# Optimization experiments

Hardware: AMD Instinct MI355X
Metric: run time of the kernel (lower is better)

## Reference

```python
import jax, jax.numpy as jnp
import numpy as np

N_EMBD = 768
N_HEAD = 12
HEAD_DIM = N_EMBD // N_HEAD


def setup_inputs() -> dict:
    key = jax.random.key(0)
    k0, k1, k2, k3, k4 = jax.random.split(key, 5)
    B, T, C = 2, 4096, N_EMBD
    x = jax.random.normal(k0, (B, T, C), dtype=jnp.float32)
    # c_attn: Linear(C, 3C); c_proj: Linear(C, C). torch Linear: y = x @ W.T + b
    s = 1.0 / np.sqrt(C)
    W_attn = jax.random.uniform(k1, (3 * C, C), dtype=jnp.float32, minval=-s, maxval=s)
    b_attn = jax.random.uniform(k2, (3 * C,), dtype=jnp.float32, minval=-s, maxval=s)
    W_proj = jax.random.uniform(k3, (C, C), dtype=jnp.float32, minval=-s, maxval=s)
    b_proj = jax.random.uniform(k4, (C,), dtype=jnp.float32, minval=-s, maxval=s)
    return {"x": x, "W_attn": W_attn, "b_attn": b_attn, "W_proj": W_proj, "b_proj": b_proj}


def reference(x, W_attn, b_attn, W_proj, b_proj):
    B, T, C = x.shape
    H, D = N_HEAD, HEAD_DIM
    qkv = x @ W_attn.T + b_attn                      # [B,T,3C]
    q, k, v = jnp.split(qkv, 3, axis=-1)
    # [B,T,C] -> [B,H,T,D]
    q = q.reshape(B, T, H, D).transpose(0, 2, 1, 3)
    k = k.reshape(B, T, H, D).transpose(0, 2, 1, 3)
    v = v.reshape(B, T, H, D).transpose(0, 2, 1, 3)
    scale = 1.0 / jnp.sqrt(jnp.asarray(D, dtype=x.dtype))
    att = jnp.einsum('bhqd,bhkd->bhqk', q, k) * scale  # [B,H,T,T]
    att = jax.nn.softmax(att, axis=-1)
    y = jnp.einsum('bhqk,bhkd->bhqd', att, v)          # [B,H,T,D]
    y = y.transpose(0, 2, 1, 3).reshape(B, T, C)
    return y @ W_proj.T + b_proj
```

## Files before the change

### kernel.cpp

```cpp
#include <hip/hip_runtime.h>
#include <stdint.h>
#include <stddef.h>

typedef __bf16 bf16_t;
typedef bf16_t bf16x4 __attribute__((ext_vector_type(4)));
typedef bf16_t bf16x8 __attribute__((ext_vector_type(8)));
typedef float  f32x4  __attribute__((ext_vector_type(4)));
typedef _Float16 f16_t;
typedef f16_t f16x2 __attribute__((ext_vector_type(2)));
typedef f16_t f16x4 __attribute__((ext_vector_type(4)));
typedef __fp16 fp16x2_raw __attribute__((ext_vector_type(2)));

__device__ __forceinline__ f16x2 pkrtz(float a, float b) {
    fp16x2_raw r = __builtin_amdgcn_cvt_pkrtz(a, b);
    union { fp16x2_raw r; f16x2 h; } u;
    u.r = r;
    return u.h;
}

#define MFMA_BF16_K32(a, b, c) __builtin_amdgcn_mfma_f32_16x16x32_bf16(a, b, c, 0, 0, 0)
#define MFMA_F16_K16(a, b, c)  __builtin_amdgcn_mfma_f32_16x16x16f16(a, b, c, 0, 0, 0)

__device__ __forceinline__ void gload_lds16(const void* g, void* l) {
    __builtin_amdgcn_global_load_lds(
        (const __attribute__((address_space(1))) void*)g,
        (__attribute__((address_space(3))) void*)l,
        16, 0, 0);
}

#define NX 1572864
#define NWA 442368
#define NWP 147456
__global__ void cvt_all(const float* __restrict__ x, const float* __restrict__ Wa,
                        const float* __restrict__ Wp, bf16_t* __restrict__ xb,
                        bf16_t* __restrict__ Wab, bf16_t* __restrict__ Wpb) {
    int i = blockIdx.x * blockDim.x + threadIdx.x;
    const float4* src; bf16_t* dst; int j;
    if (i < NX)            { src = (const float4*)x;  dst = xb;  j = i; }
    else if (i < NX + NWA) { src = (const float4*)Wa; dst = Wab; j = i - NX; }
    else                   { src = (const float4*)Wp; dst = Wpb; j = i - NX - NWA; }
    float4 f = src[j];
    bf16x4 o = { (bf16_t)f.x, (bf16_t)f.y, (bf16_t)f.z, (bf16_t)f.w };
    ((bf16x4*)dst)[j] = o;
}

template <int KDIM>
__device__ __forceinline__ void gemm_mainloop(
    const bf16_t* __restrict__ A, const bf16_t* __restrict__ Bt,
    bf16_t* As, bf16_t* Bs, int m0, int n0, int wave, int lane, f32x4 acc[4][4])
{
    const int quad = lane >> 4, l15 = lane & 15;
    const int wm = ((wave >> 1) << 6), wn = ((wave & 1) << 6);

    const int srow = (wave << 4) + (lane >> 2);
    const int sw   = (((lane & 3) ^ ((srow >> 1) & 3)) << 3);
    const bf16_t* gA = A  + (size_t)(m0 + srow) * KDIM + sw;
    const bf16_t* gB = Bt + (size_t)(n0 + srow) * KDIM + sw;
    bf16_t* lA0 = As + wave * 512;
    bf16_t* lA1 = As + 2048 + wave * 512;
    bf16_t* lB0 = Bs + wave * 512;
    bf16_t* lB1 = Bs + 2048 + wave * 512;

    const int xorv = ((quad ^ ((l15 >> 1) & 3)) << 3);

    for (int k0 = 0; k0 < KDIM; k0 += 32) {
        __syncthreads();
        gload_lds16(gA + k0,                       lA0);
        gload_lds16(gA + (size_t)64 * KDIM + k0,   lA1);
        gload_lds16(gB + k0,                       lB0);
        gload_lds16(gB + (size_t)64 * KDIM + k0,   lB1);
        __syncthreads();

        bf16x8 af[4], bfr[4];
#pragma unroll
        for (int t = 0; t < 4; t++) {
            af[t]  = *(const bf16x8*)(As + (wm + t * 16 + l15) * 32 + xorv);
            bfr[t] = *(const bf16x8*)(Bs + (wn + t * 16 + l15) * 32 + xorv);
        }
#pragma unroll
        for (int mt = 0; mt < 4; mt++)
#pragma unroll
            for (int nt = 0; nt < 4; nt++)
                acc[mt][nt] = MFMA_BF16_K32(af[mt], bfr[nt], acc[mt][nt]);
    }
}

__global__ __launch_bounds__(256) void gemm_qkv(
    const bf16_t* __restrict__ A,
    const bf16_t* __restrict__ Bt,
    const float* __restrict__ bias,
    bf16_t* __restrict__ qo, bf16_t* __restrict__ ko, f16_t* __restrict__ vo)
{
    __shared__ bf16_t As[128 * 32];
    __shared__ bf16_t Bs[128 * 32];
    const int tid = threadIdx.x, wave = tid >> 6, lane = tid & 63;
    const int quad = lane >> 4, l15 = lane & 15;
    const int m0 = blockIdx.y * 128, n0 = blockIdx.x * 128;
    f32x4 acc[4][4] = {};
    gemm_mainloop<768>(A, Bt, As, Bs, m0, n0, wave, lane, acc);

    const int wm = ((wave >> 1) << 6), wn = ((wave & 1) << 6);
#pragma unroll
    for (int nt = 0; nt < 4; nt++) {
        const int cc = n0 + wn + nt * 16 + l15;
        const float bia = bias[cc];
        const int which = cc / 768;
        const int rem = cc - which * 768;
        const int h = rem >> 6, d = rem & 63;
        if (which < 2) {
            bf16_t* dst = (which == 0) ? qo : ko;
#pragma unroll
            for (int mt = 0; mt < 4; mt++) {
#pragma unroll
                for (int r = 0; r < 4; r++) {
                    const int row = m0 + wm + mt * 16 + quad * 4 + r;
                    const int b = row >> 12, t = row & 4095;
                    dst[((size_t)(b * 12 + h) * 4096 + t) * 64 + d] =
                        (bf16_t)(acc[mt][nt][r] + bia);
                }
            }
        } else {
#pragma unroll
            for (int mt = 0; mt < 4; mt++) {
                const int row0 = m0 + wm + mt * 16 + quad * 4;
                const int b = row0 >> 12, t0 = row0 & 4095;
                f16x4 ov = { (f16_t)(acc[mt][nt][0] + bia),
                             (f16_t)(acc[mt][nt][1] + bia),
                             (f16_t)(acc[mt][nt][2] + bia),
                             (f16_t)(acc[mt][nt][3] + bia) };
                *(f16x4*)(vo + ((size_t)(b * 12 + h) * 64 + d) * 4096 + t0) = ov;
            }
        }
    }
}

__global__ __launch_bounds__(256) void gemm_proj(
    const bf16_t* __restrict__ A,
    const bf16_t* __restrict__ Bt,
    const float* __restrict__ bias,
    float* __restrict__ out)
{
    __shared__ bf16_t As[128 * 32];
    __shared__ bf16_t Bs[128 * 32];
    const int tid = threadIdx.x, wave = tid >> 6, lane = tid & 63;
    const int quad = lane >> 4, l15 = lane & 15;
    const int m0 = blockIdx.y * 128, n0 = blockIdx.x * 128;
    f32x4 acc[4][4] = {};
    gemm_mainloop<768>(A, Bt, As, Bs, m0, n0, wave, lane, acc);

    const int wm = ((wave >> 1) << 6), wn = ((wave & 1) << 6);
#pragma unroll
    for (int nt = 0; nt < 4; nt++) {
        const int cc = n0 + wn + nt * 16 + l15;
        const float bia = bias[cc];
#pragma unroll
        for (int mt = 0; mt < 4; mt++) {
#pragma unroll
            for (int r = 0; r < 4; r++) {
                const int row = m0 + wm + mt * 16 + quad * 4 + r;
                out[(size_t)row * 768 + cc] = acc[mt][nt][r] + bia;
            }
        }
    }
}

#define QSCALE 0.1803368801f
__global__ __launch_bounds__(256, 3) void attn_fwd(
    const bf16_t* __restrict__ qg, const bf16_t* __restrict__ kg,
    const f16_t* __restrict__ vtg, bf16_t* __restrict__ y)
{
    __shared__ __align__(16) char smem[36608];
    bf16_t* Ks0 = (bf16_t*)(smem);
    bf16_t* Ks1 = (bf16_t*)(smem + 8192);
    f16_t*  Vt0 = (f16_t*)(smem + 16384);
    f16_t*  Vt1 = (f16_t*)(smem + 24576);
    float*  RedA = (float*)(smem);
    float*  RedB = (float*)(smem + 17408);
    float*  Psr  = (float*)(smem + 34816);
    float*  PsT  = (float*)(smem + 35840);

    const int tid = threadIdx.x, wave = tid >> 6, lane = tid & 63;
    const int quad = lane >> 4, l15 = lane & 15;

    const int blk = blockIdx.x;
    const int xcd = blk & 7;
    const int idx = blk >> 3;
    const int hl  = idx % 3;
    const int qt  = idx / 3;
    const int bh  = xcd * 3 + hl;
    const int b = bh / 12, h = bh - b * 12;
    const size_t base = (size_t)bh * 4096 * 64;

    bf16x8 qf[4][2];
#pragma unroll
    for (int qc = 0; qc < 4; qc++) {
        const int qrow = qt * 64 + qc * 16 + l15;
        qf[qc][0] = *(const bf16x8*)(qg + base + (size_t)qrow * 64 + quad * 8);
        qf[qc][1] = *(const bf16x8*)(qg + base + (size_t)qrow * 64 + 32 + quad * 8);
#pragma unroll
        for (int j = 0; j < 8; j++) {
            qf[qc][0][j] = (bf16_t)((float)qf[qc][0][j] * QSCALE);
            qf[qc][1][j] = (bf16_t)((float)qf[qc][1][j] * QSCALE);
        }
    }

    f32x4 O[4][4] = {};
    float psum[4] = {};
    const f16x2 one2 = { (f16_t)1.0f, (f16_t)1.0f };

    const int srow8 = tid >> 3;
    const int sc8   = (tid & 7) ^ (srow8 & 7);
    const int l8 = l15 & 7;
    const int w16 = wave << 4;
    const int ksoff = (quad ^ l8) << 3;
    const int vslot = ((wave << 1) | (quad >> 1)) ^ l8;
    const int q0off = (quad & 1) * 8;

    auto stage = [&](const bf16_t* kp, const f16_t* vp, bf16_t* Kd, f16_t* Vd) {
#pragma unroll
        for (int i = 0; i < 2; i++) {
            gload_lds16(kp + (i * 32 + srow8) * 64 + sc8 * 8,           Kd + (i * 256 + tid) * 8);
            gload_lds16(vp + (size_t)(i * 32 + srow8) * 4096 + sc8 * 8, Vd + (i * 256 + tid) * 8);
        }
    };

    auto compute = [&](const bf16_t* ks, const f16_t* vs) {
        const bf16_t* kr = ks + (w16 + l15) * 64;
        bf16x8 kf0 = *(const bf16x8*)(kr + ksoff);
        bf16x8 kf1 = *(const bf16x8*)(kr + (ksoff ^ 32));
        f32x4 sc[4];
#pragma unroll
        for (int qc = 0; qc < 4; qc++) {
            f32x4 s = {};
            s = MFMA_BF16_K32(kf0, qf[qc][0], s);
            s = MFMA_BF16_K32(kf1, qf[qc][1], s);
            sc[qc] = s;
        }
        f16x4 pf[4];
#pragma unroll
        for (int qc = 0; qc < 4; qc++) {
            float e0 = __builtin_amdgcn_exp2f(sc[qc][0]);
            float e1 = __builtin_amdgcn_exp2f(sc[qc][1]);
            float e2 = __builtin_amdgcn_exp2f(sc[qc][2]);
            float e3 = __builtin_amdgcn_exp2f(sc[qc][3]);
            f16x2 lo = pkrtz(e0, e1);
            f16x2 hi = pkrtz(e2, e3);
            psum[qc] = __builtin_amdgcn_fdot2(lo, one2, psum[qc], false);
            psum[qc] = __builtin_amdgcn_fdot2(hi, one2, psum[qc], false);
            f16x4 p;
            *(f16x2*)&p = lo;
            *(((f16x2*)&p) + 1) = hi;
            pf[qc] = p;
        }
#pragma unroll
        for (int dt = 0; dt < 4; dt++) {
            const char* vr = (const char*)(vs + (dt * 16 + l15) * 64);
            f16x4 vf = *(const f16x4*)(vr + vslot * 16 + q0off);
#pragma unroll
            for (int qc = 0; qc < 4; qc++)
                O[dt][qc] = MFMA_F16_K16(vf, pf[qc], O[dt][qc]);
        }
    };

    const bf16_t* kp = kg + base;
    const f16_t*  vp = vtg + base;
    stage(kp, vp, Ks0, Vt0); kp += 4096; vp += 64;
    for (int kt = 0; kt < 64; kt += 2) {
        __syncthreads();
        stage(kp, vp, Ks1, Vt1); kp += 4096; vp += 64;
        compute(Ks0, Vt0);
        __syncthreads();
        if (kt + 2 < 64) { stage(kp, vp, Ks0, Vt0); kp += 4096; vp += 64; }
        compute(Ks1, Vt1);
    }

#pragma unroll
    for (int qc = 0; qc < 4; qc++) {
        psum[qc] += __shfl_xor(psum[qc], 16, 64);
        psum[qc] += __shfl_xor(psum[qc], 32, 64);
    }
    __syncthreads();
    if (wave == 2) {
#pragma unroll
        for (int dt = 0; dt < 4; dt++)
#pragma unroll
            for (int qc = 0; qc < 4; qc++)
                *(f32x4*)(RedA + (qc * 16 + l15) * 68 + dt * 16 + quad * 4) = O[dt][qc];
    } else if (wave == 3) {
#pragma unroll
        for (int dt = 0; dt < 4; dt++)
#pragma unroll
            for (int qc = 0; qc < 4; qc++)
                *(f32x4*)(RedB + (qc * 16 + l15) * 68 + dt * 16 + quad * 4) = O[dt][qc];
    }
    if (quad == 0) {
#pragma unroll
        for (int qc = 0; qc < 4; qc++) Psr[wave * 64 + qc * 16 + l15] = psum[qc];
    }
    __syncthreads();
    if (wave == 0) {
#pragma unroll
        for (int dt = 0; dt < 4; dt++)
#pragma unroll
            for (int qc = 0; qc < 4; qc++)
                O[dt][qc] += *(const f32x4*)(RedA + (qc * 16 + l15) * 68 + dt * 16 + quad * 4);
    } else if (wave == 1) {
#pragma unroll
        for (int dt = 0; dt < 4; dt++)
#pragma unroll
            for (int qc = 0; qc < 4; qc++)
                O[dt][qc] += *(const f32x4*)(RedB + (qc * 16 + l15) * 68 + dt * 16 + quad * 4);
    }
    __syncthreads();
    if (wave == 1) {
#pragma unroll
        for (int dt = 0; dt < 4; dt++)
#pragma unroll
            for (int qc = 0; qc < 4; qc++)
                *(f32x4*)(RedA + (qc * 16 + l15) * 68 + dt * 16 + quad * 4) = O[dt][qc];
    } else if (wave == 3) {
        PsT[lane] = Psr[lane] + Psr[64 + lane] + Psr[128 + lane] + Psr[192 + lane];
    }
    __syncthreads();
    if (wave == 0) {
#pragma unroll
        for (int qc = 0; qc < 4; qc++) {
            const float rcp = 1.0f / PsT[qc * 16 + l15];
            const int t = qt * 64 + qc * 16 + l15;
            bf16_t* yr = y + ((size_t)b * 4096 + t) * 768 + h * 64 + quad * 4;
#pragma unroll
            for (int dt = 0; dt < 4; dt++) {
                f32x4 o4 = O[dt][qc] +
                    *(const f32x4*)(RedA + (qc * 16 + l15) * 68 + dt * 16 + quad * 4);
                bf16x4 ov = { (bf16_t)(o4[0] * rcp), (bf16_t)(o4[1] * rcp),
                              (bf16_t)(o4[2] * rcp), (bf16_t)(o4[3] * rcp) };
                *(bf16x4*)(yr + dt * 16) = ov;
            }
        }
    }
}

extern "C" void kernel_launch(void* const* d_in, const int* in_sizes, int n_in,
                              void* d_out, int out_size, void* d_ws, size_t ws_size,
                              hipStream_t stream) {
    const float* x  = (const float*)d_in[0];
    const float* Wa = (const float*)d_in[1];
    const float* ba = (const float*)d_in[2];
    const float* Wp = (const float*)d_in[3];
    const float* bp = (const float*)d_in[4];
    float* out = (float*)d_out;

    char* ws = (char*)d_ws;
    bf16_t* xb  = (bf16_t*)(ws);
    bf16_t* Wab = (bf16_t*)(ws + 12582912);
    bf16_t* Wpb = (bf16_t*)(ws + 16121856);
    bf16_t* qb  = (bf16_t*)(ws + 17301504);
    bf16_t* kb  = (bf16_t*)(ws + 29884416);
    f16_t*  vtb = (f16_t*)(ws + 42467328);
    bf16_t* yb  = (bf16_t*)(ws + 55050240);

    cvt_all<<<8448, 256, 0, stream>>>(x, Wa, Wp, xb, Wab, Wpb);
    gemm_qkv <<<dim3(18, 64), 256, 0, stream>>>(xb, Wab, ba, qb, kb, vtb);
    attn_fwd <<<1536, 256, 0, stream>>>(qb, kb, vtb, yb);
    gemm_proj<<<dim3( 6, 64), 256, 0, stream>>>(yb, Wpb, bp, out);
}
```

Measured before the change: 277.7 us.

## Triple-buffer attention K/V staging and transpose GEMM operands for vector stores

The attention kernel moves from double to triple-buffered K/V tiles in LDS, using explicit vmcnt waits plus a raw s_barrier so the copy for tile t+2 stays in flight while tile t is computed. Both GEMMs swap operands (weights as A, activations as B), so each lane owns four consecutive output features and can write bf16x4, float4 or strided f16 stores and read bias as a float4. The extra buffer raises LDS use per block, which may limit occupancy under the 3-blocks-per-CU bound. The V-transpose epilogue now uses scalar strided stores instead of f16x4.

```diff
diff --git a/kernel.cpp b/kernel.cpp
--- a/kernel.cpp
+++ b/kernel.cpp
@@ -86,8 +86,8 @@
 }
 
 __global__ __launch_bounds__(256) void gemm_qkv(
-    const bf16_t* __restrict__ A,
-    const bf16_t* __restrict__ Bt,
+    const bf16_t* __restrict__ Wab,
+    const bf16_t* __restrict__ xb,
     const float* __restrict__ bias,
     bf16_t* __restrict__ qo, bf16_t* __restrict__ ko, f16_t* __restrict__ vo)
 {
@@ -95,48 +95,43 @@
     __shared__ bf16_t Bs[128 * 32];
     const int tid = threadIdx.x, wave = tid >> 6, lane = tid & 63;
     const int quad = lane >> 4, l15 = lane & 15;
-    const int m0 = blockIdx.y * 128, n0 = blockIdx.x * 128;
+    const int m0 = blockIdx.x * 128;
+    const int n0 = blockIdx.y * 128;
     f32x4 acc[4][4] = {};
-    gemm_mainloop<768>(A, Bt, As, Bs, m0, n0, wave, lane, acc);
+    gemm_mainloop<768>(Wab, xb, As, Bs, m0, n0, wave, lane, acc);
 
     const int wm = ((wave >> 1) << 6), wn = ((wave & 1) << 6);
 #pragma unroll
     for (int nt = 0; nt < 4; nt++) {
-        const int cc = n0 + wn + nt * 16 + l15;
-        const float bia = bias[cc];
-        const int which = cc / 768;
-        const int rem = cc - which * 768;
-        const int h = rem >> 6, d = rem & 63;
-        if (which < 2) {
-            bf16_t* dst = (which == 0) ? qo : ko;
-#pragma unroll
-            for (int mt = 0; mt < 4; mt++) {
-#pragma unroll
-                for (int r = 0; r < 4; r++) {
-                    const int row = m0 + wm + mt * 16 + quad * 4 + r;
-                    const int b = row >> 12, t = row & 4095;
-                    dst[((size_t)(b * 12 + h) * 4096 + t) * 64 + d] =
-                        (bf16_t)(acc[mt][nt][r] + bia);
-                }
+        const int tok = n0 + wn + nt * 16 + l15;
+        const int b = tok >> 12, tt = tok & 4095;
+#pragma unroll
+        for (int mt = 0; mt < 4; mt++) {
+            const int f0 = m0 + wm + mt * 16 + quad * 4;
+            const float4 bi = *(const float4*)(bias + f0);
+            const int which = f0 / 768;
+            const int rem = f0 - which * 768;
+            const int h = rem >> 6, d0 = rem & 63;
+            const float v0 = acc[mt][nt][0] + bi.x, v1 = acc[mt][nt][1] + bi.y;
+            const float v2 = acc[mt][nt][2] + bi.z, v3 = acc[mt][nt][3] + bi.w;
+            if (which < 2) {
+                bf16_t* dst = (which == 0) ? qo : ko;
+                bf16x4 ov = { (bf16_t)v0, (bf16_t)v1, (bf16_t)v2, (bf16_t)v3 };
+                *(bf16x4*)(dst + ((size_t)(b * 12 + h) * 4096 + tt) * 64 + d0) = ov;
+            } else {
+                f16_t* vd = vo + ((size_t)(b * 12 + h) * 64 + d0) * 4096 + tt;
+                vd[0]         = (f16_t)v0;
+                vd[4096]      = (f16_t)v1;
+                vd[2 * 4096]  = (f16_t)v2;
+                vd[3 * 4096]  = (f16_t)v3;
             }
-        } else {
-#pragma unroll
-            for (int mt = 0; mt < 4; mt++) {
-                const int row0 = m0 + wm + mt * 16 + quad * 4;
-                const int b = row0 >> 12, t0 = row0 & 4095;
-                f16x4 ov = { (f16_t)(acc[mt][nt][0] + bia),
-                             (f16_t)(acc[mt][nt][1] + bia),
-                             (f16_t)(acc[mt][nt][2] + bia),
-                             (f16_t)(acc[mt][nt][3] + bia) };
-                *(f16x4*)(vo + ((size_t)(b * 12 + h) * 64 + d) * 4096 + t0) = ov;
-            }
         }
     }
 }
 
 __global__ __launch_bounds__(256) void gemm_proj(
-    const bf16_t* __restrict__ A,
-    const bf16_t* __restrict__ Bt,
+    const bf16_t* __restrict__ Wpb,
+    const bf16_t* __restrict__ yb,
     const float* __restrict__ bias,
     float* __restrict__ out)
 {
@@ -144,40 +139,39 @@
     __shared__ bf16_t Bs[128 * 32];
     const int tid = threadIdx.x, wave = tid >> 6, lane = tid & 63;
     const int quad = lane >> 4, l15 = lane & 15;
-    const int m0 = blockIdx.y * 128, n0 = blockIdx.x * 128;
+    const int m0 = blockIdx.x * 128;
+    const int n0 = blockIdx.y * 128;
     f32x4 acc[4][4] = {};
-    gemm_mainloop<768>(A, Bt, As, Bs, m0, n0, wave, lane, acc);
+    gemm_mainloop<768>(Wpb, yb, As, Bs, m0, n0, wave, lane, acc);
 
     const int wm = ((wave >> 1) << 6), wn = ((wave & 1) << 6);
 #pragma unroll
     for (int nt = 0; nt < 4; nt++) {
-        const int cc = n0 + wn + nt * 16 + l15;
-        const float bia = bias[cc];
+        const int tok = n0 + wn + nt * 16 + l15;
 #pragma unroll
         for (int mt = 0; mt < 4; mt++) {
-#pragma unroll
-            for (int r = 0; r < 4; r++) {
-                const int row = m0 + wm + mt * 16 + quad * 4 + r;
-                out[(size_t)row * 768 + cc] = acc[mt][nt][r] + bia;
-            }
+            const int f0 = m0 + wm + mt * 16 + quad * 4;
+            const float4 bi = *(const float4*)(bias + f0);
+            float4 o = { acc[mt][nt][0] + bi.x, acc[mt][nt][1] + bi.y,
+                         acc[mt][nt][2] + bi.z, acc[mt][nt][3] + bi.w };
+            *(float4*)(out + (size_t)tok * 768 + f0) = o;
         }
     }
 }
 
 #define QSCALE 0.1803368801f
+#define WAIT_VM4 0x0F74
+#define WAIT_VM0 0x0F70
 __global__ __launch_bounds__(256, 3) void attn_fwd(
     const bf16_t* __restrict__ qg, const bf16_t* __restrict__ kg,
     const f16_t* __restrict__ vtg, bf16_t* __restrict__ y)
 {
-    __shared__ __align__(16) char smem[36608];
-    bf16_t* Ks0 = (bf16_t*)(smem);
-    bf16_t* Ks1 = (bf16_t*)(smem + 8192);
-    f16_t*  Vt0 = (f16_t*)(smem + 16384);
-    f16_t*  Vt1 = (f16_t*)(smem + 24576);
-    float*  RedA = (float*)(smem);
-    float*  RedB = (float*)(smem + 17408);
-    float*  Psr  = (float*)(smem + 34816);
-    float*  PsT  = (float*)(smem + 35840);
+    __shared__ __align__(16) bf16_t K0s[4096], K1s[4096], K2s[4096];
+    __shared__ __align__(16) f16_t  V0s[4096], V1s[4096], V2s[4096];
+    __shared__ __align__(16) float  Psr[256];
+    __shared__ float PsT[64];
+    float* RedA = (float*)K0s;
+    float* RedB = (float*)(((char*)K0s) + 17408);
 
     const int tid = threadIdx.x, wave = tid >> 6, lane = tid & 63;
     const int quad = lane >> 4, l15 = lane & 15;
@@ -190,6 +184,8 @@
     const int bh  = xcd * 3 + hl;
     const int b = bh / 12, h = bh - b * 12;
     const size_t base = (size_t)bh * 4096 * 64;
+    const bf16_t* kgt = kg + base;
+    const f16_t*  vgt = vtg + base;
 
     bf16x8 qf[4][2];
 #pragma unroll
@@ -216,7 +212,9 @@
     const int vslot = ((wave << 1) | (quad >> 1)) ^ l8;
     const int q0off = (quad & 1) * 8;
 
-    auto stage = [&](const bf16_t* kp, const f16_t* vp, bf16_t* Kd, f16_t* Vd) {
+    auto stageT = [&](int t, bf16_t* Kd, f16_t* Vd) {
+        const bf16_t* kp = kgt + (size_t)t * 4096;
+        const f16_t*  vp = vgt + t * 64;
 #pragma unroll
         for (int i = 0; i < 2; i++) {
             gload_lds16(kp + (i * 32 + srow8) * 64 + sc8 * 8,           Kd + (i * 256 + tid) * 8);
@@ -262,17 +260,27 @@
         }
     };
 
-    const bf16_t* kp = kg + base;
-    const f16_t*  vp = vtg + base;
-    stage(kp, vp, Ks0, Vt0); kp += 4096; vp += 64;
-    for (int kt = 0; kt < 64; kt += 2) {
-        __syncthreads();
-        stage(kp, vp, Ks1, Vt1); kp += 4096; vp += 64;
-        compute(Ks0, Vt0);
-        __syncthreads();
-        if (kt + 2 < 64) { stage(kp, vp, Ks0, Vt0); kp += 4096; vp += 64; }
-        compute(Ks1, Vt1);
-    }
+    stageT(0, K0s, V0s);
+    stageT(1, K1s, V1s);
+    for (int t = 0; t < 63; t += 3) {
+        __builtin_amdgcn_s_waitcnt(WAIT_VM4);
+        __builtin_amdgcn_s_barrier();
+        compute(K0s, V0s);
+        stageT(t + 2, K2s, V2s);
+
+        __builtin_amdgcn_s_waitcnt(WAIT_VM4);
+        __builtin_amdgcn_s_barrier();
+        compute(K1s, V1s);
+        stageT(t + 3, K0s, V0s);
+
+        __builtin_amdgcn_s_waitcnt(WAIT_VM4);
+        __builtin_amdgcn_s_barrier();
+        compute(K2s, V2s);
+        stageT(t + 4 < 64 ? t + 4 : 63, K1s, V1s);
+    }
+    __builtin_amdgcn_s_waitcnt(WAIT_VM0);
+    __builtin_amdgcn_s_barrier();
+    compute(K0s, V0s);
 
 #pragma unroll
     for (int qc = 0; qc < 4; qc++) {
@@ -360,7 +368,7 @@
     bf16_t* yb  = (bf16_t*)(ws + 55050240);
 
     cvt_all<<<8448, 256, 0, stream>>>(x, Wa, Wp, xb, Wab, Wpb);
-    gemm_qkv <<<dim3(18, 64), 256, 0, stream>>>(xb, Wab, ba, qb, kb, vtb);
+    gemm_qkv <<<dim3(18, 64), 256, 0, stream>>>(Wab, xb, ba, qb, kb, vtb);
     attn_fwd <<<1536, 256, 0, stream>>>(qb, kb, vtb, yb);
-    gemm_proj<<<dim3( 6, 64), 256, 0, stream>>>(yb, Wpb, bp, out);
-}
+    gemm_proj<<<dim3( 6, 64), 256, 0, stream>>>(Wpb, yb, bp, out);
+}
```

After: 300.8 us. 1.08x slower.
